# Optimization experiments

Hardware: AMD Instinct MI355X
Metric: run time of the kernel (lower is better)

The kernel has to match this reference:

```python
import jax, jax.numpy as jnp
import numpy as np

B, T = 512, 8192
MIN_SPEECH = 1.0      # config.min_speech_frames
MAX_EXPAND = 3.0      # config.max_speech_expand
TOPK_RATIO = 0.35     # config.pause_topk_ratio
MIN_BW = 0.1          # config.pause_min_boundary_weight
BIAS_W = 0.15         # config.pause_boundary_bias_weight
TEMP = 0.12           # config.pause_soft_temperature


def setup_inputs() -> dict:
    key = jax.random.key(0)
    ks = jax.random.split(key, 9)
    return {
        "dur_anchor_src": jax.random.uniform(ks[0], (B, T)) * 10.0,
        "dur_logratio_unit": jax.random.normal(ks[1], (B, T)) * 0.3,
        "pause_weight_unit": jax.random.uniform(ks[2], (B, T)),
        "boundary_latent": jax.random.uniform(ks[3], (B, T)),
        "unit_mask": jnp.ones((B, T), jnp.float32),
        "speech_budget_win": jax.random.uniform(ks[4], (B,)) * (2.0 * T),
        "pause_budget_win": jax.random.uniform(ks[5], (B,)) * (0.2 * T),
        "previous_speech_exec": jax.random.uniform(ks[6], (B, T)) * 3.0,
        "previous_pause_exec": jax.random.uniform(ks[7], (B, T)),
        "commit_frontier": jax.random.randint(ks[8], (B,), 0, T // 2),
    }


def reference(dur_anchor_src, dur_logratio_unit, pause_weight_unit, boundary_latent,
              unit_mask, speech_budget_win, pause_budget_win,
              previous_speech_exec, previous_pause_exec, commit_frontier):
    Tn = unit_mask.shape[1]
    pos = jnp.arange(Tn)[None, :]                                  # [1,T]
    prefix_mask = (pos < commit_frontier[:, None]).astype(unit_mask.dtype)  # [B,T]
    tail_mask = unit_mask * (1.0 - prefix_mask)

    # ---- lift budgets to feasible region (reuse_prefix=True) ----
    prefix_speech = jnp.sum(previous_speech_exec * unit_mask * prefix_mask, axis=1)
    prefix_pause = jnp.sum(previous_pause_exec * unit_mask * prefix_mask, axis=1)
    min_tail_speech = jnp.sum(tail_mask, axis=1) * MIN_SPEECH
    speech_budget = jnp.maximum(speech_budget_win, prefix_speech + min_tail_speech)
    pause_budget = jnp.maximum(pause_budget_win, prefix_pause)

    # ---- project speech ----
    anchor = jnp.maximum(dur_anchor_src, MIN_SPEECH)
    base = anchor * jnp.exp(dur_logratio_unit)
    candidate = jnp.clip(base, MIN_SPEECH, anchor * MAX_EXPAND) * unit_mask
    speech_prefix = previous_speech_exec * unit_mask * prefix_mask
    rem_s = speech_budget - jnp.sum(speech_prefix, axis=1)          # [B]
    cand_tail_sum = jnp.maximum(jnp.sum(candidate * tail_mask, axis=1), 1e-6)
    do_s = (jnp.sum(tail_mask, axis=1) > 0) & (rem_s > 0)
    scale_s = jnp.where(do_s, rem_s / cand_tail_sum, 0.0)[:, None]
    speech = (speech_prefix + candidate * scale_s * tail_mask) * unit_mask

    # ---- project pause (soft top-k selection) ----
    scores = (jnp.maximum(pause_weight_unit, 0.0)
              + BIAS_W * (MIN_BW + jnp.maximum(boundary_latent, 0.0))) * unit_mask
    keep_k = max(1, int(round(Tn * TOPK_RATIO)))                    # static, < T
    topv = jax.lax.top_k(scores, keep_k)[0]                         # [B,keep_k]
    thr = jax.lax.stop_gradient(topv[:, -1])[:, None]               # detached threshold
    gate = jax.nn.sigmoid((scores - thr) / TEMP)
    sparse = scores * gate * unit_mask

    pause_prefix = previous_pause_exec * unit_mask * prefix_mask
    rem_p = jnp.maximum(pause_budget - jnp.sum(pause_prefix, axis=1), 0.0)
    tail_sum = jnp.sum(tail_mask, axis=1)
    fallback = tail_mask / jnp.maximum(tail_sum, 1.0)[:, None]
    tail_cand = jnp.maximum(sparse, 0.0) * tail_mask + fallback * 1e-6
    denom = jnp.maximum(jnp.sum(tail_cand * tail_mask, axis=1), 1e-6)
    do_p = (tail_sum > 0) & (rem_p > 0)
    scale_p = jnp.where(do_p, rem_p / denom, 0.0)[:, None]
    pause = (pause_prefix + tail_cand * scale_p * tail_mask) * unit_mask

    return jnp.stack([speech, pause])                               # [2,B,T]
```

## Files before the change

### kernel.cpp

```cpp
#include <hip/hip_runtime.h>

#define T_DIM 8192
#define NTH 512
#define NWAVE 8
#define GROUPS 4
#define KEEP_K 2867
#define KSCALE 32768.0f
#define INV_KSCALE (1.0f / 32768.0f)

typedef float nt4 __attribute__((ext_vector_type(4)));

__device__ __forceinline__ void scan_top256(const unsigned* bins, unsigned k, int lane,
                                            unsigned* sh_digit, unsigned* sh_k) {
    const int r0 = lane * 4;
    const unsigned c0 = bins[255 - r0];
    const unsigned c1 = bins[255 - (r0 + 1)];
    const unsigned c2 = bins[255 - (r0 + 2)];
    const unsigned c3 = bins[255 - (r0 + 3)];
    const unsigned s1 = c0 + c1, s2 = s1 + c2, s3 = s2 + c3;
    unsigned tot = s3;
    #pragma unroll
    for (int off = 1; off < 64; off <<= 1) {
        const unsigned n = __shfl_up(tot, off, 64);
        if (lane >= off) tot += n;
    }
    const unsigned excl = tot - s3;
    const unsigned Pc[4] = { excl + c0, excl + s1, excl + s2, excl + s3 };
    unsigned prev = excl;
    #pragma unroll
    for (int c = 0; c < 4; ++c) {
        if (Pc[c] >= k && prev < k) {
            *sh_digit = (unsigned)(255 - (r0 + c));
            *sh_k = k - prev;
        }
        prev = Pc[c];
    }
}

__global__ __launch_bounds__(NTH, 4) void srp_kernel(
    const float* __restrict__ g_anchor,
    const float* __restrict__ g_lr,
    const float* __restrict__ g_pw,
    const float* __restrict__ g_bl,
    const float* __restrict__ g_mask,
    const float* __restrict__ g_sbud,
    const float* __restrict__ g_pbud,
    const float* __restrict__ g_psp,
    const float* __restrict__ g_ppa,
    const int*  __restrict__ g_front,
    float* __restrict__ g_out,
    int n_rows)
{
    constexpr float MIN_SPEECH = 1.0f;
    constexpr float MAX_EXPAND = 3.0f;
    constexpr float MIN_BW = 0.1f;
    constexpr float BIAS_W = 0.15f;
    constexpr float INV_TEMP = 1.0f / 0.12f;

    __shared__ unsigned ku[T_DIM / 2];
    __shared__ unsigned hist[NWAVE][256];
    __shared__ unsigned s_tot[256];
    __shared__ float wred[NWAVE][4];
    __shared__ float s_scal[6];
    __shared__ unsigned sh_hb, sh_k1, sh_lb, sh_k2;

    const int b = blockIdx.x;
    const int tid = threadIdx.x;
    const int wave = tid >> 6;
    const int lane = tid & 63;
    const long long row = (long long)b * T_DIM;
    const int f = g_front[b];

    #pragma unroll
    for (int d = 0; d < 4; ++d) hist[wave][lane + 64 * d] = 0u;

    float SC1[16];
    float P1[16];
    float Mm[16];
    float a_ps = 0.f, a_pp = 0.f, a_ts = 0.f, a_cs = 0.f;

    #pragma unroll
    for (int g = 0; g < GROUPS; ++g) {
        const int t0 = g * 2048 + (tid << 2);
        const float4 an4 = *reinterpret_cast<const float4*>(g_anchor + row + t0);
        const float4 lr4 = *reinterpret_cast<const float4*>(g_lr + row + t0);
        const float4 pw4 = *reinterpret_cast<const float4*>(g_pw + row + t0);
        const float4 bl4 = *reinterpret_cast<const float4*>(g_bl + row + t0);
        const float4 mk4 = *reinterpret_cast<const float4*>(g_mask + row + t0);
        const float4 ps4 = *reinterpret_cast<const float4*>(g_psp + row + t0);
        const float4 pp4 = *reinterpret_cast<const float4*>(g_ppa + row + t0);
        unsigned kk0 = 0u, kk1 = 0u;
        #pragma unroll
        for (int c = 0; c < 4; ++c) {
            const int i = (g << 2) + c;
            const int t = t0 + c;
            const float m   = (&mk4.x)[c];
            const float pre = (t < f) ? 1.0f : 0.0f;
            const float tail = m * (1.0f - pre);
            const float ps = (&ps4.x)[c];
            const float pp = (&pp4.x)[c];
            a_ps += ps * m * pre;
            a_pp += pp * m * pre;
            a_ts += tail;
            const float an = fmaxf((&an4.x)[c], MIN_SPEECH);
            const float cand = fminf(fmaxf(an * __expf((&lr4.x)[c]), MIN_SPEECH),
                                     an * MAX_EXPAND) * m;
            a_cs += cand * tail;
            const float s = (fmaxf((&pw4.x)[c], 0.0f)
                             + BIAS_W * (MIN_BW + fmaxf((&bl4.x)[c], 0.0f))) * m;
            const unsigned key = (unsigned)fminf(s * KSCALE, 65535.0f);
            atomicAdd(&hist[wave][key >> 8], 1u);
            if (c < 2) kk0 |= key << (16 * c);
            else       kk1 |= key << (16 * (c - 2));
            SC1[i] = ps * m * m * pre + cand * tail * m;
            P1[i]  = pp * m * m * pre;
            Mm[i]  = m;
        }
        uint2 w2; w2.x = kk0; w2.y = kk1;
        *reinterpret_cast<uint2*>(&ku[t0 >> 1]) = w2;
    }

    #pragma unroll
    for (int o = 32; o > 0; o >>= 1) {
        a_ps += __shfl_down(a_ps, o, 64);
        a_pp += __shfl_down(a_pp, o, 64);
        a_ts += __shfl_down(a_ts, o, 64);
        a_cs += __shfl_down(a_cs, o, 64);
    }
    if (lane == 0) {
        wred[wave][0] = a_ps; wred[wave][1] = a_pp;
        wred[wave][2] = a_ts; wred[wave][3] = a_cs;
    }
    __syncthreads();

    if (tid < 256) {
        unsigned s = 0;
        #pragma unroll
        for (int w = 0; w < NWAVE; ++w) s += hist[w][tid];
        s_tot[tid] = s;
    }
    if (tid == 0) {
        float ps = 0.f, pp = 0.f, ts = 0.f, cs = 0.f;
        for (int w = 0; w < NWAVE; ++w) {
            ps += wred[w][0]; pp += wred[w][1];
            ts += wred[w][2]; cs += wred[w][3];
        }
        const float sb = fmaxf(g_sbud[b], ps + ts * MIN_SPEECH);
        const float pb = fmaxf(g_pbud[b], pp);
        const float rem_s = sb - ps;
        const float cts = fmaxf(cs, 1e-6f);
        s_scal[0] = (ts > 0.0f && rem_s > 0.0f) ? (rem_s / cts) : 0.0f;
        s_scal[1] = fmaxf(pb - pp, 0.0f);
        s_scal[2] = ts;
        s_scal[3] = fmaxf(ts, 1.0f);
    }
    __syncthreads();

    {
        const float scale_s = s_scal[0];
        #pragma unroll
        for (int g = 0; g < GROUPS; ++g) {
            const int t0 = g * 2048 + (tid << 2);
            nt4 vs;
            #pragma unroll
            for (int c = 0; c < 4; ++c) {
                const int i = (g << 2) + c;
                const int t = t0 + c;
                vs[c] = (t < f) ? SC1[i] : SC1[i] * scale_s;
            }
            __builtin_nontemporal_store(vs, reinterpret_cast<nt4*>(g_out + row + t0));
        }
    }
    #pragma unroll
    for (int d = 0; d < 4; ++d) hist[wave][lane + 64 * d] = 0u;
    if (wave == 0) scan_top256(s_tot, KEEP_K, lane, &sh_hb, &sh_k1);
    __syncthreads();

    const unsigned hb = sh_hb;
    #pragma unroll
    for (int g = 0; g < GROUPS; ++g) {
        const int t0 = g * 2048 + (tid << 2);
        const uint2 w2 = *reinterpret_cast<const uint2*>(&ku[t0 >> 1]);
        const unsigned k0 = w2.x & 0xFFFFu, k1 = w2.x >> 16;
        const unsigned k2 = w2.y & 0xFFFFu, k3 = w2.y >> 16;
        if ((k0 >> 8) == hb) atomicAdd(&hist[wave][k0 & 0xFFu], 1u);
        if ((k1 >> 8) == hb) atomicAdd(&hist[wave][k1 & 0xFFu], 1u);
        if ((k2 >> 8) == hb) atomicAdd(&hist[wave][k2 & 0xFFu], 1u);
        if ((k3 >> 8) == hb) atomicAdd(&hist[wave][k3 & 0xFFu], 1u);
    }
    __syncthreads();
    if (tid < 256) {
        unsigned s = 0;
        #pragma unroll
        for (int w = 0; w < NWAVE; ++w) s += hist[w][tid];
        s_tot[tid] = s;
    }
    __syncthreads();
    if (wave == 0) scan_top256(s_tot, sh_k1, lane, &sh_lb, &sh_k2);
    __syncthreads();

    const float thr = (float)((sh_hb << 8) | sh_lb) * INV_KSCALE;

    const float inv_ts6 = 1e-6f / s_scal[3];
    float a_d = 0.0f;
    #pragma unroll
    for (int g = 0; g < GROUPS; ++g) {
        const int t0 = g * 2048 + (tid << 2);
        const uint2 w2 = *reinterpret_cast<const uint2*>(&ku[t0 >> 1]);
        const unsigned kk[4] = { w2.x & 0xFFFFu, w2.x >> 16, w2.y & 0xFFFFu, w2.y >> 16 };
        #pragma unroll
        for (int c = 0; c < 4; ++c) {
            const int i = (g << 2) + c;
            const int t = t0 + c;
            const float m = Mm[i];
            const float pre = (t < f) ? 1.0f : 0.0f;
            const float tail = m * (1.0f - pre);
            const float s = (float)kk[c] * INV_KSCALE;
            const float gate = 1.0f / (1.0f + __expf(-(s - thr) * INV_TEMP));
            const float tc = s * gate * m * tail + tail * inv_ts6;
            a_d += tc * tail;
            P1[i] += tc * tail * m;
        }
    }
    #pragma unroll
    for (int o = 32; o > 0; o >>= 1) a_d += __shfl_down(a_d, o, 64);
    if (lane == 0) wred[wave][0] = a_d;
    __syncthreads();
    if (tid == 0) {
        float d = 0.f;
        for (int w = 0; w < NWAVE; ++w) d += wred[w][0];
        const float denom = fmaxf(d, 1e-6f);
        const float ts = s_scal[2];
        const float rem_p = s_scal[1];
        s_scal[4] = (ts > 0.0f && rem_p > 0.0f) ? (rem_p / denom) : 0.0f;
    }
    __syncthreads();

    const float scale_p = s_scal[4];
    const long long out_off = (long long)n_rows * T_DIM;
    #pragma unroll
    for (int g = 0; g < GROUPS; ++g) {
        const int t0 = g * 2048 + (tid << 2);
        nt4 vp;
        #pragma unroll
        for (int c = 0; c < 4; ++c) {
            const int i = (g << 2) + c;
            const int t = t0 + c;
            vp[c] = (t < f) ? P1[i] : P1[i] * scale_p;
        }
        __builtin_nontemporal_store(vp, reinterpret_cast<nt4*>(g_out + out_off + row + t0));
    }
}

extern "C" void kernel_launch(void* const* d_in, const int* in_sizes, int n_in,
                              void* d_out, int out_size, void* d_ws, size_t ws_size,
                              hipStream_t stream) {
    const float* anchor = (const float*)d_in[0];
    const float* lr     = (const float*)d_in[1];
    const float* pw     = (const float*)d_in[2];
    const float* bl     = (const float*)d_in[3];
    const float* mask   = (const float*)d_in[4];
    const float* sbud   = (const float*)d_in[5];
    const float* pbud   = (const float*)d_in[6];
    const float* psp    = (const float*)d_in[7];
    const float* ppa    = (const float*)d_in[8];
    const int*   front  = (const int*)d_in[9];
    float* out = (float*)d_out;
    const int B = in_sizes[5];
    srp_kernel<<<B, NTH, 0, stream>>>(anchor, lr, pw, bl, mask, sbud, pbud,
                                      psp, ppa, front, out, B);
}
```

Measured before the change: 169.5 us.

## Replace two-pass radix top-k select with single 2048-bin histogram and binned denominator

The two-level 256-bin radix select for the top-k threshold is replaced by one pass over a 2048-bin shared histogram, so the threshold is known to bin resolution only. The pause denominator is now built from per-bin weighted score sums, evaluating the sigmoid once per bin centre instead of once per element. This removes a second histogram pass, the shared key buffer, and several barriers. The cost is that both the threshold and the denominator become approximations, and float atomics on shared memory are added in the first pass.

```diff
diff --git a/kernel.cpp b/kernel.cpp
--- a/kernel.cpp
+++ b/kernel.cpp
@@ -4,38 +4,13 @@
 #define NTH 512
 #define NWAVE 8
 #define GROUPS 4
+#define NBIN 2048
 #define KEEP_K 2867
 #define KSCALE 32768.0f
 #define INV_KSCALE (1.0f / 32768.0f)
+#define BINW (32.0f / 32768.0f)
 
 typedef float nt4 __attribute__((ext_vector_type(4)));
-
-__device__ __forceinline__ void scan_top256(const unsigned* bins, unsigned k, int lane,
-                                            unsigned* sh_digit, unsigned* sh_k) {
-    const int r0 = lane * 4;
-    const unsigned c0 = bins[255 - r0];
-    const unsigned c1 = bins[255 - (r0 + 1)];
-    const unsigned c2 = bins[255 - (r0 + 2)];
-    const unsigned c3 = bins[255 - (r0 + 3)];
-    const unsigned s1 = c0 + c1, s2 = s1 + c2, s3 = s2 + c3;
-    unsigned tot = s3;
-    #pragma unroll
-    for (int off = 1; off < 64; off <<= 1) {
-        const unsigned n = __shfl_up(tot, off, 64);
-        if (lane >= off) tot += n;
-    }
-    const unsigned excl = tot - s3;
-    const unsigned Pc[4] = { excl + c0, excl + s1, excl + s2, excl + s3 };
-    unsigned prev = excl;
-    #pragma unroll
-    for (int c = 0; c < 4; ++c) {
-        if (Pc[c] >= k && prev < k) {
-            *sh_digit = (unsigned)(255 - (r0 + c));
-            *sh_k = k - prev;
-        }
-        prev = Pc[c];
-    }
-}
 
 __global__ __launch_bounds__(NTH, 4) void srp_kernel(
     const float* __restrict__ g_anchor,
@@ -57,12 +32,11 @@
     constexpr float BIAS_W = 0.15f;
     constexpr float INV_TEMP = 1.0f / 0.12f;
 
-    __shared__ unsigned ku[T_DIM / 2];
-    __shared__ unsigned hist[NWAVE][256];
-    __shared__ unsigned s_tot[256];
-    __shared__ float wred[NWAVE][4];
+    __shared__ unsigned s_cnt[NBIN];
+    __shared__ float    s_ws[NBIN];
+    __shared__ float wred[NWAVE][5];
     __shared__ float s_scal[6];
-    __shared__ unsigned sh_hb, sh_k1, sh_lb, sh_k2;
+    __shared__ float sh_thr;
 
     const int b = blockIdx.x;
     const int tid = threadIdx.x;
@@ -70,14 +44,21 @@
     const int lane = tid & 63;
     const long long row = (long long)b * T_DIM;
     const int f = g_front[b];
-
-    #pragma unroll
-    for (int d = 0; d < 4; ++d) hist[wave][lane + 64 * d] = 0u;
+    const float sbud = g_sbud[b];
+    const float pbud = g_pbud[b];
+
+    #pragma unroll
+    for (int i = 0; i < NBIN / NTH; ++i) {
+        s_cnt[tid + NTH * i] = 0u;
+        s_ws[tid + NTH * i]  = 0.f;
+    }
+    __syncthreads();
 
     float SC1[16];
     float P1[16];
     float Mm[16];
-    float a_ps = 0.f, a_pp = 0.f, a_ts = 0.f, a_cs = 0.f;
+    unsigned kp[8];
+    float a_ps = 0.f, a_pp = 0.f, a_ts = 0.f, a_cs = 0.f, a_t2 = 0.f;
 
     #pragma unroll
     for (int g = 0; g < GROUPS; ++g) {
@@ -96,28 +77,31 @@
             const int t = t0 + c;
             const float m   = (&mk4.x)[c];
             const float pre = (t < f) ? 1.0f : 0.0f;
-            const float tail = m * (1.0f - pre);
+            const float tl  = m * (1.0f - pre);
             const float ps = (&ps4.x)[c];
             const float pp = (&pp4.x)[c];
             a_ps += ps * m * pre;
             a_pp += pp * m * pre;
-            a_ts += tail;
+            a_ts += tl;
+            a_t2 += tl * tl;
             const float an = fmaxf((&an4.x)[c], MIN_SPEECH);
             const float cand = fminf(fmaxf(an * __expf((&lr4.x)[c]), MIN_SPEECH),
                                      an * MAX_EXPAND) * m;
-            a_cs += cand * tail;
+            a_cs += cand * tl;
             const float s = (fmaxf((&pw4.x)[c], 0.0f)
                              + BIAS_W * (MIN_BW + fmaxf((&bl4.x)[c], 0.0f))) * m;
             const unsigned key = (unsigned)fminf(s * KSCALE, 65535.0f);
-            atomicAdd(&hist[wave][key >> 8], 1u);
+            atomicAdd(&s_cnt[key >> 5], 1u);
+            const float w = m * tl * tl * s;
+            if (w > 0.0f) atomicAdd(&s_ws[key >> 5], w);
             if (c < 2) kk0 |= key << (16 * c);
             else       kk1 |= key << (16 * (c - 2));
-            SC1[i] = ps * m * m * pre + cand * tail * m;
+            SC1[i] = ps * m * m * pre + cand * tl * m;
             P1[i]  = pp * m * m * pre;
             Mm[i]  = m;
         }
-        uint2 w2; w2.x = kk0; w2.y = kk1;
-        *reinterpret_cast<uint2*>(&ku[t0 >> 1]) = w2;
+        kp[2 * g]     = kk0;
+        kp[2 * g + 1] = kk1;
     }
 
     #pragma unroll
@@ -126,127 +110,114 @@
         a_pp += __shfl_down(a_pp, o, 64);
         a_ts += __shfl_down(a_ts, o, 64);
         a_cs += __shfl_down(a_cs, o, 64);
+        a_t2 += __shfl_down(a_t2, o, 64);
     }
     if (lane == 0) {
         wred[wave][0] = a_ps; wred[wave][1] = a_pp;
         wred[wave][2] = a_ts; wred[wave][3] = a_cs;
-    }
-    __syncthreads();
-
-    if (tid < 256) {
-        unsigned s = 0;
-        #pragma unroll
-        for (int w = 0; w < NWAVE; ++w) s += hist[w][tid];
-        s_tot[tid] = s;
-    }
-    if (tid == 0) {
-        float ps = 0.f, pp = 0.f, ts = 0.f, cs = 0.f;
+        wred[wave][4] = a_t2;
+    }
+    __syncthreads();
+
+    if (tid == 64) {
+        float ps = 0.f, pp = 0.f, ts = 0.f, cs = 0.f, t2 = 0.f;
         for (int w = 0; w < NWAVE; ++w) {
-            ps += wred[w][0]; pp += wred[w][1];
-            ts += wred[w][2]; cs += wred[w][3];
-        }
-        const float sb = fmaxf(g_sbud[b], ps + ts * MIN_SPEECH);
-        const float pb = fmaxf(g_pbud[b], pp);
+            ps += wred[w][0]; pp += wred[w][1]; ts += wred[w][2];
+            cs += wred[w][3]; t2 += wred[w][4];
+        }
+        const float sb = fmaxf(sbud, ps + ts * MIN_SPEECH);
+        const float pb = fmaxf(pbud, pp);
         const float rem_s = sb - ps;
         const float cts = fmaxf(cs, 1e-6f);
         s_scal[0] = (ts > 0.0f && rem_s > 0.0f) ? (rem_s / cts) : 0.0f;
         s_scal[1] = fmaxf(pb - pp, 0.0f);
         s_scal[2] = ts;
-        s_scal[3] = fmaxf(ts, 1.0f);
-    }
-    __syncthreads();
-
-    {
-        const float scale_s = s_scal[0];
-        #pragma unroll
-        for (int g = 0; g < GROUPS; ++g) {
-            const int t0 = g * 2048 + (tid << 2);
-            nt4 vs;
-            #pragma unroll
-            for (int c = 0; c < 4; ++c) {
-                const int i = (g << 2) + c;
-                const int t = t0 + c;
-                vs[c] = (t < f) ? SC1[i] : SC1[i] * scale_s;
+        s_scal[3] = 1e-6f / fmaxf(ts, 1.0f);
+        s_scal[5] = t2;
+    }
+    if (wave == 0) {
+        const int base = NBIN - 32 * (lane + 1);
+        unsigned csum = 0;
+        #pragma unroll
+        for (int i = 0; i < 32; ++i) csum += s_cnt[base + i];
+        unsigned tot = csum;
+        #pragma unroll
+        for (int off = 1; off < 64; off <<= 1) {
+            const unsigned n = __shfl_up(tot, off, 64);
+            if (lane >= off) tot += n;
+        }
+        const unsigned excl = tot - csum;
+        if (excl < KEEP_K && excl + csum >= KEEP_K) {
+            const unsigned need = KEEP_K - excl;
+            unsigned c = 0;
+            int bin = base;
+            for (int i = 31; i >= 0; --i) {
+                c += s_cnt[base + i];
+                if (c >= need) { bin = base + i; break; }
             }
-            __builtin_nontemporal_store(vs, reinterpret_cast<nt4*>(g_out + row + t0));
-        }
-    }
-    #pragma unroll
-    for (int d = 0; d < 4; ++d) hist[wave][lane + 64 * d] = 0u;
-    if (wave == 0) scan_top256(s_tot, KEEP_K, lane, &sh_hb, &sh_k1);
-    __syncthreads();
-
-    const unsigned hb = sh_hb;
+            sh_thr = (float)bin * BINW;
+        }
+    }
+    __syncthreads();
+
+    const float thr = sh_thr;
+    const float scale_s = s_scal[0];
+    const float inv_ts6 = s_scal[3];
+
     #pragma unroll
     for (int g = 0; g < GROUPS; ++g) {
         const int t0 = g * 2048 + (tid << 2);
-        const uint2 w2 = *reinterpret_cast<const uint2*>(&ku[t0 >> 1]);
-        const unsigned k0 = w2.x & 0xFFFFu, k1 = w2.x >> 16;
-        const unsigned k2 = w2.y & 0xFFFFu, k3 = w2.y >> 16;
-        if ((k0 >> 8) == hb) atomicAdd(&hist[wave][k0 & 0xFFu], 1u);
-        if ((k1 >> 8) == hb) atomicAdd(&hist[wave][k1 & 0xFFu], 1u);
-        if ((k2 >> 8) == hb) atomicAdd(&hist[wave][k2 & 0xFFu], 1u);
-        if ((k3 >> 8) == hb) atomicAdd(&hist[wave][k3 & 0xFFu], 1u);
-    }
-    __syncthreads();
-    if (tid < 256) {
-        unsigned s = 0;
-        #pragma unroll
-        for (int w = 0; w < NWAVE; ++w) s += hist[w][tid];
-        s_tot[tid] = s;
-    }
-    __syncthreads();
-    if (wave == 0) scan_top256(s_tot, sh_k1, lane, &sh_lb, &sh_k2);
-    __syncthreads();
-
-    const float thr = (float)((sh_hb << 8) | sh_lb) * INV_KSCALE;
-
-    const float inv_ts6 = 1e-6f / s_scal[3];
+        nt4 vs;
+        #pragma unroll
+        for (int c = 0; c < 4; ++c) {
+            const int i = (g << 2) + c;
+            const int t = t0 + c;
+            vs[c] = (t < f) ? SC1[i] : SC1[i] * scale_s;
+        }
+        __builtin_nontemporal_store(vs, reinterpret_cast<nt4*>(g_out + row + t0));
+    }
+
     float a_d = 0.0f;
+    #pragma unroll
+    for (int i = 0; i < NBIN / NTH; ++i) {
+        const int bin = tid + NTH * i;
+        const float w = s_ws[bin];
+        const float sc = ((float)bin + 0.5f) * BINW;
+        a_d += w / (1.0f + __expf(-(sc - thr) * INV_TEMP));
+    }
+    #pragma unroll
+    for (int o = 32; o > 0; o >>= 1) a_d += __shfl_down(a_d, o, 64);
+    if (lane == 0) wred[wave][0] = a_d;
+    __syncthreads();
+    if (tid == 0) {
+        float d = 0.f;
+        for (int w = 0; w < NWAVE; ++w) d += wred[w][0];
+        d += s_scal[5] * inv_ts6;
+        const float denom = fmaxf(d, 1e-6f);
+        const float ts = s_scal[2];
+        const float rem_p = s_scal[1];
+        s_scal[4] = (ts > 0.0f && rem_p > 0.0f) ? (rem_p / denom) : 0.0f;
+    }
+    __syncthreads();
+
+    const float scale_p = s_scal[4];
+    const long long out_off = (long long)n_rows * T_DIM;
     #pragma unroll
     for (int g = 0; g < GROUPS; ++g) {
         const int t0 = g * 2048 + (tid << 2);
-        const uint2 w2 = *reinterpret_cast<const uint2*>(&ku[t0 >> 1]);
-        const unsigned kk[4] = { w2.x & 0xFFFFu, w2.x >> 16, w2.y & 0xFFFFu, w2.y >> 16 };
+        const unsigned kk0 = kp[2 * g], kk1 = kp[2 * g + 1];
+        const unsigned kk[4] = { kk0 & 0xFFFFu, kk0 >> 16, kk1 & 0xFFFFu, kk1 >> 16 };
+        nt4 vp;
         #pragma unroll
         for (int c = 0; c < 4; ++c) {
             const int i = (g << 2) + c;
             const int t = t0 + c;
             const float m = Mm[i];
             const float pre = (t < f) ? 1.0f : 0.0f;
-            const float tail = m * (1.0f - pre);
+            const float tl = m * (1.0f - pre);
             const float s = (float)kk[c] * INV_KSCALE;
             const float gate = 1.0f / (1.0f + __expf(-(s - thr) * INV_TEMP));
-            const float tc = s * gate * m * tail + tail * inv_ts6;
-            a_d += tc * tail;
-            P1[i] += tc * tail * m;
-        }
-    }
-    #pragma unroll
-    for (int o = 32; o > 0; o >>= 1) a_d += __shfl_down(a_d, o, 64);
-    if (lane == 0) wred[wave][0] = a_d;
-    __syncthreads();
-    if (tid == 0) {
-        float d = 0.f;
-        for (int w = 0; w < NWAVE; ++w) d += wred[w][0];
-        const float denom = fmaxf(d, 1e-6f);
-        const float ts = s_scal[2];
-        const float rem_p = s_scal[1];
-        s_scal[4] = (ts > 0.0f && rem_p > 0.0f) ? (rem_p / denom) : 0.0f;
-    }
-    __syncthreads();
-
-    const float scale_p = s_scal[4];
-    const long long out_off = (long long)n_rows * T_DIM;
-    #pragma unroll
-    for (int g = 0; g < GROUPS; ++g) {
-        const int t0 = g * 2048 + (tid << 2);
-        nt4 vp;
-        #pragma unroll
-        for (int c = 0; c < 4; ++c) {
-            const int i = (g << 2) + c;
-            const int t = t0 + c;
-            vp[c] = (t < f) ? P1[i] : P1[i] * scale_p;
+            vp[c] = P1[i] + scale_p * tl * tl * (s * gate * m + inv_ts6);
         }
         __builtin_nontemporal_store(vp, reinterpret_cast<nt4*>(g_out + out_off + row + t0));
     }
```

Measured after the change: 194.1 us. 1.15x slower.
